# Kernel optimization log

Measured on AMD Instinct MI355X. Metric: run time of the kernel, lower is better.

Reference implementation:

```python
import jax, jax.numpy as jnp
import numpy as np

B, T, H, K = 16, 8192, 256, 128
HQ = H // 4
NEG_INF = -jnp.inf


def setup_inputs() -> dict:
    key = jax.random.key(0)
    k1, k2, k3, k4, k5, k6, k7 = jax.random.split(key, 7)
    projected = jax.random.normal(k1, (B, T, H), dtype=jnp.float32)
    boundaries = jnp.sort(jax.random.randint(k2, (B, K, 2), 0, T), axis=-1)
    slot_mask = jax.random.randint(k3, (B, K), 0, 2, dtype=jnp.int32)
    # score_fn params: Linear(H, H//4) -> Tanh -> Linear(H//4, 1)
    s1 = 1.0 / np.sqrt(H)
    s2 = 1.0 / np.sqrt(HQ)
    W1 = jax.random.uniform(k4, (H, HQ), jnp.float32, -s1, s1)
    b1 = jax.random.uniform(k5, (HQ,), jnp.float32, -s1, s1)
    W2 = jax.random.uniform(k6, (HQ, 1), jnp.float32, -s2, s2)
    b2 = jax.random.uniform(k7, (1,), jnp.float32, -s2, s2)
    return {"projected": projected, "boundaries": boundaries, "slot_mask": slot_mask,
            "W1": W1, "b1": b1, "W2": W2, "b2": b2}


def reference(projected, boundaries, slot_mask, W1, b1, W2, b2):
    # scores: [B, T]
    h = jnp.tanh(projected @ W1 + b1)          # [B,T,HQ]
    scores = (h @ W2 + b2)[..., 0]             # [B,T]

    tidx = jnp.arange(T)[None, :, None]         # [1,T,1]
    starts = boundaries[:, None, :, 0]          # [B,1,K]
    ends = boundaries[:, None, :, 1]            # [B,1,K]
    in_slot = (tidx >= starts) & (tidx < ends) & (slot_mask[:, None, :] > 0)  # [B,T,K]

    # masked softmax over T, safe for fully-masked slots (torch yields 0 via masked_fill)
    s = scores[:, :, None]                      # [B,T,1] broadcast over K
    m = jnp.max(jnp.where(in_slot, s, NEG_INF), axis=1, keepdims=True)  # [B,1,K]
    m_safe = jnp.where(jnp.isfinite(m), m, 0.0)
    num = jnp.where(in_slot, jnp.exp(s - m_safe), 0.0)                  # [B,T,K]
    den = jnp.sum(num, axis=1, keepdims=True)                           # [B,1,K]
    w = num / jnp.where(den > 0, den, 1.0)                              # [B,T,K]

    return jnp.einsum('btk,bth->bkh', w, projected)                     # [B,K,H]
```

## Files before the change

kernel.cpp:

```cpp
#include <hip/hip_runtime.h>
#include <hip/hip_bf16.h>

#define BB 16
#define TT 8192
#define HH 256
#define KK 128
#define HQ 64

#define PTILE 128
#define NCH 32

typedef __attribute__((ext_vector_type(8))) short short8;
typedef __attribute__((ext_vector_type(4))) float f32x4;

__device__ inline unsigned short bf16_rne(float f) {
  unsigned u = __float_as_uint(f);
  unsigned r = u + 0x7FFF + ((u >> 16) & 1);
  return (unsigned short)(r >> 16);
}
__device__ inline float bf16_to_f(unsigned short h) {
  return __uint_as_float(((unsigned)h) << 16);
}

__global__ void prep_kernel(const float* __restrict__ W1,
                            unsigned short* __restrict__ Wp)
{
  const int tid = threadIdx.x;
  for (int r = 0; r < 64; ++r) {
    int f = r * 256 + tid;
    int e = f & 7;
    int l = (f >> 3) & 63;
    int n = (f >> 9) & 3;
    int s = f >> 11;
    int k = s * 32 + ((l >> 4) * 8) + e;
    int j = n * 16 + (l & 15);
    float w = W1[k * HQ + j];
    unsigned short hi = bf16_rne(w);
    unsigned short lo = bf16_rne(w - bf16_to_f(hi));
    Wp[f] = hi;
    Wp[16384 + f] = lo;
  }
}

__global__ __launch_bounds__(256, 2) void scores_mfma_kernel(
    const float* __restrict__ proj, const unsigned short* __restrict__ Wp,
    const float* __restrict__ b1, const float* __restrict__ W2,
    const float* __restrict__ b2, float* __restrict__ scores)
{
  __shared__ unsigned short Ahi[32][264];
  __shared__ unsigned short Alo[32][264];
  __shared__ float part[4][32];

  const int tid = threadIdx.x;
  const long long tile = blockIdx.x;
  const float4* src4 = (const float4*)(proj + tile * (32LL * HH));

  #pragma unroll
  for (int r = 0; r < 8; ++r) {
    int f = r * 256 + tid;
    int t = f >> 6;
    int c = f & 63;
    float4 v = src4[f];
    unsigned short h0 = bf16_rne(v.x), h1 = bf16_rne(v.y);
    unsigned short h2 = bf16_rne(v.z), h3 = bf16_rne(v.w);
    ushort4 hv = make_ushort4(h0, h1, h2, h3);
    ushort4 lv = make_ushort4(bf16_rne(v.x - bf16_to_f(h0)),
                              bf16_rne(v.y - bf16_to_f(h1)),
                              bf16_rne(v.z - bf16_to_f(h2)),
                              bf16_rne(v.w - bf16_to_f(h3)));
    *(ushort4*)&Ahi[t][4 * c] = hv;
    *(ushort4*)&Alo[t][4 * c] = lv;
  }
  __syncthreads();

  const int w = tid >> 6;
  const int l = tid & 63;
  const int g = l >> 4;
  const int c = l & 15;

  f32x4 acc[2];
  #pragma unroll
  for (int m = 0; m < 2; ++m) acc[m] = (f32x4){0.f, 0.f, 0.f, 0.f};

  const short8* wp_hi = (const short8*)Wp;
  const short8* wp_lo = (const short8*)(Wp + 16384);

  #pragma unroll
  for (int s = 0; s < 8; ++s) {
    short8 bhi = wp_hi[(s * 4 + w) * 64 + l];
    short8 blo = wp_lo[(s * 4 + w) * 64 + l];
    #pragma unroll
    for (int m = 0; m < 2; ++m) {
      short8 ahi = *(const short8*)&Ahi[m * 16 + c][s * 32 + g * 8];
      short8 alo = *(const short8*)&Alo[m * 16 + c][s * 32 + g * 8];
      acc[m] = __builtin_amdgcn_mfma_f32_16x16x32_bf16(ahi, bhi, acc[m], 0, 0, 0);
      acc[m] = __builtin_amdgcn_mfma_f32_16x16x32_bf16(ahi, blo, acc[m], 0, 0, 0);
      acc[m] = __builtin_amdgcn_mfma_f32_16x16x32_bf16(alo, bhi, acc[m], 0, 0, 0);
    }
  }

  const int j = w * 16 + c;
  const float b1j = b1[j];
  const float w2j = W2[j];

  #pragma unroll
  for (int m = 0; m < 2; ++m) {
    #pragma unroll
    for (int r = 0; r < 4; ++r) {
      float x = tanhf(acc[m][r] + b1j) * w2j;
      x += __shfl_xor(x, 1);
      x += __shfl_xor(x, 2);
      x += __shfl_xor(x, 4);
      x += __shfl_xor(x, 8);
      if (c == r) part[w][m * 16 + g * 4 + r] = x;
    }
  }
  __syncthreads();

  if (tid < 32) {
    float s = part[0][tid] + part[1][tid] + part[2][tid] + part[3][tid] + b2[0];
    scores[tile * 32 + tid] = s;
  }
}

__global__ __launch_bounds__(256) void slotstats_kernel(
    const float* __restrict__ scores, const int* __restrict__ boundaries,
    const int* __restrict__ slot_mask, float* __restrict__ m_arr,
    float* __restrict__ invden)
{
  const int slot = blockIdx.x;
  const int b = slot >> 7;
  const int tid = threadIdx.x;
  const int st = boundaries[slot * 2 + 0];
  const int en = boundaries[slot * 2 + 1];
  const int mk = slot_mask[slot];
  __shared__ float red[4];

  if (mk <= 0 || en <= st) {
    if (tid == 0) { m_arr[slot] = 0.f; invden[slot] = 0.f; }
    return;
  }
  const float* sc = scores + (long long)b * TT;

  float mx = -3.4e38f;
  for (int t = st + tid; t < en; t += 256) mx = fmaxf(mx, sc[t]);
  #pragma unroll
  for (int o = 32; o > 0; o >>= 1) mx = fmaxf(mx, __shfl_xor(mx, o));
  if ((tid & 63) == 0) red[tid >> 6] = mx;
  __syncthreads();
  mx = fmaxf(fmaxf(red[0], red[1]), fmaxf(red[2], red[3]));
  __syncthreads();

  float se = 0.f;
  for (int t = st + tid; t < en; t += 256) se += expf(sc[t] - mx);
  #pragma unroll
  for (int o = 32; o > 0; o >>= 1) se += __shfl_xor(se, o);
  if ((tid & 63) == 0) red[tid >> 6] = se;
  __syncthreads();
  if (tid == 0) {
    m_arr[slot] = mx;
    invden[slot] = 1.f / (red[0] + red[1] + red[2] + red[3]);
  }
}

__global__ __launch_bounds__(256, 4) void pool_kernel(
    const float* __restrict__ proj, const float* __restrict__ scores,
    const int* __restrict__ boundaries, const float* __restrict__ m_arr,
    const float* __restrict__ invden, float* __restrict__ out)
{
  __shared__ float s_lds[PTILE];
  __shared__ __align__(16) float w_lds[NCH][PTILE];
  __shared__ int   act_k[KK];
  __shared__ float act_m[KK], act_i[KK];
  __shared__ int   act_s[KK], act_e[KK];
  __shared__ int   nact;

  const int tid = threadIdx.x;
  const int b = blockIdx.y;
  const int t0 = blockIdx.x * PTILE;

  if (tid == 0) nact = 0;
  __syncthreads();

  if (tid < PTILE) s_lds[tid] = scores[(long long)b * TT + t0 + tid];
  if (tid < KK) {
    const int k = tid;
    const int st = boundaries[(b * KK + k) * 2 + 0];
    const int en = boundaries[(b * KK + k) * 2 + 1];
    const float inv = invden[b * KK + k];
    if (inv > 0.f && st < t0 + PTILE && en > t0) {
      int pos = atomicAdd(&nact, 1);
      act_k[pos] = k;
      act_m[pos] = m_arr[b * KK + k];
      act_i[pos] = inv;
      act_s[pos] = st;
      act_e[pos] = en;
    }
  }
  __syncthreads();
  const int na = nact;
  const float* __restrict__ pb = proj + ((long long)b * TT + t0) * HH + tid;

  for (int c = 0; c < na; c += NCH) {
    #pragma unroll
    for (int q = 0; q < 16; ++q) {
      int f = q * 256 + tid;
      int it = f >> 7;
      int tk = f & 127;
      float w = 0.f;
      int ss = c + it;
      if (ss < na) {
        int tg = t0 + tk;
        if (tg >= act_s[ss] && tg < act_e[ss])
          w = expf(s_lds[tk] - act_m[ss]) * act_i[ss];
      }
      w_lds[it][tk] = w;
    }
    __syncthreads();

    float a[NCH];
    #pragma unroll
    for (int s = 0; s < NCH; ++s) a[s] = 0.f;

    for (int t4 = 0; t4 < PTILE; t4 += 4) {
      float p0 = pb[(t4 + 0) * HH];
      float p1 = pb[(t4 + 1) * HH];
      float p2 = pb[(t4 + 2) * HH];
      float p3 = pb[(t4 + 3) * HH];
      #pragma unroll
      for (int s = 0; s < NCH; ++s) {
        float4 wv = *(const float4*)&w_lds[s][t4];
        a[s] = fmaf(wv.x, p0, a[s]);
        a[s] = fmaf(wv.y, p1, a[s]);
        a[s] = fmaf(wv.z, p2, a[s]);
        a[s] = fmaf(wv.w, p3, a[s]);
      }
    }

    #pragma unroll
    for (int s = 0; s < NCH; ++s) {
      if (c + s < na)
        atomicAdd(out + ((long long)(b * KK + act_k[c + s])) * HH + tid, a[s]);
    }
    __syncthreads();
  }
}

extern "C" void kernel_launch(void* const* d_in, const int* in_sizes, int n_in,
                              void* d_out, int out_size, void* d_ws, size_t ws_size,
                              hipStream_t stream)
{
  const float* proj       = (const float*)d_in[0];
  const int*   boundaries = (const int*)d_in[1];
  const int*   slot_mask  = (const int*)d_in[2];
  const float* W1         = (const float*)d_in[3];
  const float* b1         = (const float*)d_in[4];
  const float* W2         = (const float*)d_in[5];
  const float* b2         = (const float*)d_in[6];
  float* out = (float*)d_out;

  unsigned short* Wp = (unsigned short*)d_ws;
  float* scores = (float*)(Wp + 32768);
  float* m_arr  = scores + (size_t)BB * TT;
  float* invden = m_arr + BB * KK;

  hipMemsetAsync(d_out, 0, (size_t)out_size * sizeof(float), stream);

  prep_kernel<<<dim3(1), dim3(256), 0, stream>>>(W1, Wp);
  scores_mfma_kernel<<<dim3(BB * TT / 32), dim3(256), 0, stream>>>(
      proj, Wp, b1, W2, b2, scores);
  slotstats_kernel<<<dim3(BB * KK), dim3(256), 0, stream>>>(
      scores, boundaries, slot_mask, m_arr, invden);
  pool_kernel<<<dim3(TT / PTILE, BB), dim3(256), 0, stream>>>(
      proj, scores, boundaries, m_arr, invden, out);
}
```

Baseline: 337.3 us.

## Move pooling einsum to split-bf16 MFMA and enlarge scores tile

```diff
diff --git a/kernel.cpp b/kernel.cpp
--- a/kernel.cpp
+++ b/kernel.cpp
@@ -7,8 +7,7 @@
 #define KK 128
 #define HQ 64
 
-#define PTILE 128
-#define NCH 32
+#define PT 64
 
 typedef __attribute__((ext_vector_type(8))) short short8;
 typedef __attribute__((ext_vector_type(4))) float f32x4;
@@ -25,21 +24,17 @@
 __global__ void prep_kernel(const float* __restrict__ W1,
                             unsigned short* __restrict__ Wp)
 {
-  const int tid = threadIdx.x;
-  for (int r = 0; r < 64; ++r) {
-    int f = r * 256 + tid;
-    int e = f & 7;
-    int l = (f >> 3) & 63;
-    int n = (f >> 9) & 3;
-    int s = f >> 11;
-    int k = s * 32 + ((l >> 4) * 8) + e;
-    int j = n * 16 + (l & 15);
-    float w = W1[k * HQ + j];
-    unsigned short hi = bf16_rne(w);
-    unsigned short lo = bf16_rne(w - bf16_to_f(hi));
-    Wp[f] = hi;
-    Wp[16384 + f] = lo;
-  }
+  int f = blockIdx.x * 256 + threadIdx.x;
+  int e = f & 7;
+  int l = (f >> 3) & 63;
+  int n = (f >> 9) & 3;
+  int s = f >> 11;
+  int k = s * 32 + ((l >> 4) * 8) + e;
+  int j = n * 16 + (l & 15);
+  float w = W1[k * HQ + j];
+  unsigned short hi = bf16_rne(w);
+  Wp[f] = hi;
+  Wp[16384 + f] = bf16_rne(w - bf16_to_f(hi));
 }
 
 __global__ __launch_bounds__(256, 2) void scores_mfma_kernel(
@@ -47,29 +42,27 @@
     const float* __restrict__ b1, const float* __restrict__ W2,
     const float* __restrict__ b2, float* __restrict__ scores)
 {
-  __shared__ unsigned short Ahi[32][264];
-  __shared__ unsigned short Alo[32][264];
-  __shared__ float part[4][32];
+  __shared__ unsigned short Ahi[64][264];
+  __shared__ unsigned short Alo[64][264];
+  __shared__ float part[4][64];
 
   const int tid = threadIdx.x;
   const long long tile = blockIdx.x;
-  const float4* src4 = (const float4*)(proj + tile * (32LL * HH));
-
-  #pragma unroll
-  for (int r = 0; r < 8; ++r) {
+  const float4* src4 = (const float4*)(proj + tile * (64LL * HH));
+
+  #pragma unroll
+  for (int r = 0; r < 16; ++r) {
     int f = r * 256 + tid;
     int t = f >> 6;
     int c = f & 63;
     float4 v = src4[f];
     unsigned short h0 = bf16_rne(v.x), h1 = bf16_rne(v.y);
     unsigned short h2 = bf16_rne(v.z), h3 = bf16_rne(v.w);
-    ushort4 hv = make_ushort4(h0, h1, h2, h3);
-    ushort4 lv = make_ushort4(bf16_rne(v.x - bf16_to_f(h0)),
-                              bf16_rne(v.y - bf16_to_f(h1)),
-                              bf16_rne(v.z - bf16_to_f(h2)),
-                              bf16_rne(v.w - bf16_to_f(h3)));
-    *(ushort4*)&Ahi[t][4 * c] = hv;
-    *(ushort4*)&Alo[t][4 * c] = lv;
+    *(ushort4*)&Ahi[t][4 * c] = make_ushort4(h0, h1, h2, h3);
+    *(ushort4*)&Alo[t][4 * c] = make_ushort4(bf16_rne(v.x - bf16_to_f(h0)),
+                                             bf16_rne(v.y - bf16_to_f(h1)),
+                                             bf16_rne(v.z - bf16_to_f(h2)),
+                                             bf16_rne(v.w - bf16_to_f(h3)));
   }
   __syncthreads();
 
@@ -78,9 +71,9 @@
   const int g = l >> 4;
   const int c = l & 15;
 
-  f32x4 acc[2];
-  #pragma unroll
-  for (int m = 0; m < 2; ++m) acc[m] = (f32x4){0.f, 0.f, 0.f, 0.f};
+  f32x4 acc[4];
+  #pragma unroll
+  for (int m = 0; m < 4; ++m) acc[m] = (f32x4){0.f, 0.f, 0.f, 0.f};
 
   const short8* wp_hi = (const short8*)Wp;
   const short8* wp_lo = (const short8*)(Wp + 16384);
@@ -90,7 +83,7 @@
     short8 bhi = wp_hi[(s * 4 + w) * 64 + l];
     short8 blo = wp_lo[(s * 4 + w) * 64 + l];
     #pragma unroll
-    for (int m = 0; m < 2; ++m) {
+    for (int m = 0; m < 4; ++m) {
       short8 ahi = *(const short8*)&Ahi[m * 16 + c][s * 32 + g * 8];
       short8 alo = *(const short8*)&Alo[m * 16 + c][s * 32 + g * 8];
       acc[m] = __builtin_amdgcn_mfma_f32_16x16x32_bf16(ahi, bhi, acc[m], 0, 0, 0);
@@ -104,7 +97,7 @@
   const float w2j = W2[j];
 
   #pragma unroll
-  for (int m = 0; m < 2; ++m) {
+  for (int m = 0; m < 4; ++m) {
     #pragma unroll
     for (int r = 0; r < 4; ++r) {
       float x = tanhf(acc[m][r] + b1j) * w2j;
@@ -117,9 +110,9 @@
   }
   __syncthreads();
 
-  if (tid < 32) {
+  if (tid < 64) {
     float s = part[0][tid] + part[1][tid] + part[2][tid] + part[3][tid] + b2[0];
-    scores[tile * 32 + tid] = s;
+    scores[tile * 64 + tid] = s;
   }
 }
 
@@ -163,13 +156,14 @@
   }
 }
 
-__global__ __launch_bounds__(256, 4) void pool_kernel(
+__global__ __launch_bounds__(512, 4) void pool_mfma_kernel(
     const float* __restrict__ proj, const float* __restrict__ scores,
     const int* __restrict__ boundaries, const float* __restrict__ m_arr,
     const float* __restrict__ invden, float* __restrict__ out)
 {
-  __shared__ float s_lds[PTILE];
-  __shared__ __align__(16) float w_lds[NCH][PTILE];
+  __shared__ unsigned short Bhi[256 * 64];
+  __shared__ unsigned short Blo[256 * 64];
+  __shared__ float s_lds[PT];
   __shared__ int   act_k[KK];
   __shared__ float act_m[KK], act_i[KK];
   __shared__ int   act_s[KK], act_e[KK];
@@ -177,18 +171,18 @@
 
   const int tid = threadIdx.x;
   const int b = blockIdx.y;
-  const int t0 = blockIdx.x * PTILE;
+  const int t0 = blockIdx.x * PT;
 
   if (tid == 0) nact = 0;
   __syncthreads();
 
-  if (tid < PTILE) s_lds[tid] = scores[(long long)b * TT + t0 + tid];
+  if (tid < PT) s_lds[tid] = scores[(long long)b * TT + t0 + tid];
   if (tid < KK) {
     const int k = tid;
     const int st = boundaries[(b * KK + k) * 2 + 0];
     const int en = boundaries[(b * KK + k) * 2 + 1];
     const float inv = invden[b * KK + k];
-    if (inv > 0.f && st < t0 + PTILE && en > t0) {
+    if (inv > 0.f && st < t0 + PT && en > t0) {
       int pos = atomicAdd(&nact, 1);
       act_k[pos] = k;
       act_m[pos] = m_arr[b * KK + k];
@@ -199,50 +193,106 @@
   }
   __syncthreads();
   const int na = nact;
-  const float* __restrict__ pb = proj + ((long long)b * TT + t0) * HH + tid;
-
-  for (int c = 0; c < na; c += NCH) {
-    #pragma unroll
-    for (int q = 0; q < 16; ++q) {
-      int f = q * 256 + tid;
-      int it = f >> 7;
-      int tk = f & 127;
-      float w = 0.f;
-      int ss = c + it;
-      if (ss < na) {
-        int tg = t0 + tk;
-        if (tg >= act_s[ss] && tg < act_e[ss])
-          w = expf(s_lds[tk] - act_m[ss]) * act_i[ss];
+  if (na == 0) return;
+
+  {
+    const int h = tid & 255;
+    const int half = tid >> 8;
+    const float* __restrict__ pcol =
+        proj + ((long long)b * TT + t0 + half * 32) * HH + h;
+    unsigned short* bh = &Bhi[h * 64];
+    unsigned short* bl = &Blo[h * 64];
+    const int hs = h & 7;
+    #pragma unroll
+    for (int o = 0; o < 4; ++o) {
+      float v[8];
+      #pragma unroll
+      for (int i = 0; i < 8; ++i) v[i] = pcol[(o * 8 + i) * HH];
+      short8 hv, lv;
+      #pragma unroll
+      for (int i = 0; i < 8; ++i) {
+        unsigned short hi = bf16_rne(v[i]);
+        hv[i] = (short)hi;
+        lv[i] = (short)bf16_rne(v[i] - bf16_to_f(hi));
       }
-      w_lds[it][tk] = w;
-    }
-    __syncthreads();
-
-    float a[NCH];
-    #pragma unroll
-    for (int s = 0; s < NCH; ++s) a[s] = 0.f;
-
-    for (int t4 = 0; t4 < PTILE; t4 += 4) {
-      float p0 = pb[(t4 + 0) * HH];
-      float p1 = pb[(t4 + 1) * HH];
-      float p2 = pb[(t4 + 2) * HH];
-      float p3 = pb[(t4 + 3) * HH];
-      #pragma unroll
-      for (int s = 0; s < NCH; ++s) {
-        float4 wv = *(const float4*)&w_lds[s][t4];
-        a[s] = fmaf(wv.x, p0, a[s]);
-        a[s] = fmaf(wv.y, p1, a[s]);
-        a[s] = fmaf(wv.z, p2, a[s]);
-        a[s] = fmaf(wv.w, p3, a[s]);
+      int cch = half * 4 + o;
+      *(short8*)&bh[(cch ^ hs) << 3] = hv;
+      *(short8*)&bl[(cch ^ hs) << 3] = lv;
+    }
+  }
+  __syncthreads();
+
+  const int l = tid & 63;
+  const int w = tid >> 6;
+  const int g = l >> 4;
+  const int cl = l & 15;
+  const int hbase = w * 32;
+
+  for (int c0 = 0; c0 < na; c0 += 32) {
+    f32x4 acc[2][2];
+    #pragma unroll
+    for (int m = 0; m < 2; ++m)
+      #pragma unroll
+      for (int nt = 0; nt < 2; ++nt) acc[m][nt] = (f32x4){0.f, 0.f, 0.f, 0.f};
+
+    #pragma unroll
+    for (int ksub = 0; ksub < 2; ++ksub) {
+      float4 sv0 = *(const float4*)&s_lds[ksub * 32 + g * 8];
+      float4 sv1 = *(const float4*)&s_lds[ksub * 32 + g * 8 + 4];
+      float sv[8] = {sv0.x, sv0.y, sv0.z, sv0.w, sv1.x, sv1.y, sv1.z, sv1.w};
+
+      short8 ahi[2], alo[2];
+      #pragma unroll
+      for (int m = 0; m < 2; ++m) {
+        if (c0 + m * 16 < na) {
+          int sidx = c0 + m * 16 + cl;
+          bool act = sidx < na;
+          int ix = act ? sidx : 0;
+          float am = act_m[ix], ai = act_i[ix];
+          int as = act_s[ix], ae = act_e[ix];
+          #pragma unroll
+          for (int e = 0; e < 8; ++e) {
+            int t = t0 + ksub * 32 + g * 8 + e;
+            float wgt = 0.f;
+            if (act && t >= as && t < ae) wgt = expf(sv[e] - am) * ai;
+            unsigned short hi = bf16_rne(wgt);
+            ahi[m][e] = (short)hi;
+            alo[m][e] = (short)bf16_rne(wgt - bf16_to_f(hi));
+          }
+        }
       }
-    }
-
-    #pragma unroll
-    for (int s = 0; s < NCH; ++s) {
-      if (c + s < na)
-        atomicAdd(out + ((long long)(b * KK + act_k[c + s])) * HH + tid, a[s]);
-    }
-    __syncthreads();
+
+      #pragma unroll
+      for (int nt = 0; nt < 2; ++nt) {
+        int hr = hbase + nt * 16 + cl;
+        int cch = ksub * 4 + g;
+        int off = hr * 64 + ((cch ^ (hr & 7)) << 3);
+        short8 bhv = *(const short8*)&Bhi[off];
+        short8 blv = *(const short8*)&Blo[off];
+        #pragma unroll
+        for (int m = 0; m < 2; ++m) {
+          if (c0 + m * 16 < na) {
+            acc[m][nt] = __builtin_amdgcn_mfma_f32_16x16x32_bf16(ahi[m], bhv, acc[m][nt], 0, 0, 0);
+            acc[m][nt] = __builtin_amdgcn_mfma_f32_16x16x32_bf16(ahi[m], blv, acc[m][nt], 0, 0, 0);
+            acc[m][nt] = __builtin_amdgcn_mfma_f32_16x16x32_bf16(alo[m], bhv, acc[m][nt], 0, 0, 0);
+          }
+        }
+      }
+    }
+
+    #pragma unroll
+    for (int m = 0; m < 2; ++m) {
+      #pragma unroll
+      for (int r = 0; r < 4; ++r) {
+        int sc_i = c0 + m * 16 + g * 4 + r;
+        if (sc_i < na) {
+          long long obase = ((long long)(b * KK + act_k[sc_i])) * HH;
+          #pragma unroll
+          for (int nt = 0; nt < 2; ++nt)
+            atomicAdd(out + obase + hbase + nt * 16 + cl, acc[m][nt][r]);
+        }
+      }
+    }
   }
 }
 
@@ -266,11 +316,11 @@
 
   hipMemsetAsync(d_out, 0, (size_t)out_size * sizeof(float), stream);
 
-  prep_kernel<<<dim3(1), dim3(256), 0, stream>>>(W1, Wp);
-  scores_mfma_kernel<<<dim3(BB * TT / 32), dim3(256), 0, stream>>>(
+  prep_kernel<<<dim3(64), dim3(256), 0, stream>>>(W1, Wp);
+  scores_mfma_kernel<<<dim3(BB * TT / 64), dim3(256), 0, stream>>>(
       proj, Wp, b1, W2, b2, scores);
   slotstats_kernel<<<dim3(BB * KK), dim3(256), 0, stream>>>(
       scores, boundaries, slot_mask, m_arr, invden);
-  pool_kernel<<<dim3(TT / PTILE, BB), dim3(256), 0, stream>>>(
+  pool_mfma_kernel<<<dim3(TT / PT, BB), dim3(512), 0, stream>>>(
       proj, scores, boundaries, m_arr, invden, out);
 }
```

After: 312.4 us. -7.4%, faster.
